# Kernel optimization log

Measured on AMD Instinct MI355X. Metric: run time of the kernel, lower is better.

Reference implementation:

```python
import jax, jax.numpy as jnp
import numpy as np
import math

B, T1, T2, T3, D = 8, 32, 32, 16, 512
L, DL = 20, 128


def setup_inputs() -> dict:
    key = jax.random.key(0)
    ks = jax.random.split(key, 16)
    s = lambda fan: 1.0 / math.sqrt(fan)
    return {
        "f_c": jax.random.normal(ks[0], (B, T1, T2, T3, D), jnp.float32),
        "f_w": jax.random.normal(ks[1], (B, L, D), jnp.float32),
        "f_s": jax.random.normal(ks[2], (B, D), jnp.float32),
        "f_m": jax.random.normal(ks[3], (B, T1, T2, D), jnp.float32),
        "Wc_down": jax.random.normal(ks[4], (DL, D), jnp.float32) * s(D),
        "bc_down": jnp.zeros((DL,), jnp.float32),
        "Ww": jax.random.normal(ks[5], (DL, D), jnp.float32) * s(D),
        "bw": jnp.zeros((DL,), jnp.float32),
        "Ws": jax.random.normal(ks[6], (DL, D), jnp.float32) * s(D),
        "bs": jnp.zeros((DL,), jnp.float32),
        "Wq": jax.random.normal(ks[7], (DL, DL), jnp.float32) * s(DL),
        "bq": jnp.zeros((DL,), jnp.float32),
        "Wk": jax.random.normal(ks[8], (DL, DL), jnp.float32) * s(DL),
        "bk": jnp.zeros((DL,), jnp.float32),
        "Wc_up": jax.random.normal(ks[9], (D, DL), jnp.float32) * s(DL),
        "bc_up": jnp.zeros((D,), jnp.float32),
    }


def reference(f_c, f_w, f_s, f_m, Wc_down, bc_down, Ww, bw, Ws, bs,
              Wq, bq, Wk, bk, Wc_up, bc_up):
    inv_sqrt_dl = 1.0 / math.sqrt(DL)
    # 1x1 conv projections == per-position linear layers
    f_c_hat = jnp.einsum('bxyzd,ld->bxyzl', f_c, Wc_down) + bc_down  # [B,T1,T2,T3,dl]
    f_w_hat = f_w @ Ww.T + bw                                        # [B,L,dl]
    f_s_hat = f_s @ Ws.T + bs                                        # [B,dl]
    # Content attention: query from map, key/value from words
    q = f_c_hat @ Wq.T + bq                                          # [B,T1,T2,T3,dl]
    k = f_w_hat @ Wk.T + bk                                          # [B,L,dl]
    scores = jnp.einsum('bxyzd,bld->bxyzl', q, k) * inv_sqrt_dl
    attn = jax.nn.softmax(scores, axis=-1)
    f_caq = jnp.einsum('bxyzl,bld->bxyzd', attn, f_w_hat)            # [B,T1,T2,T3,dl]
    # Gate with sentence feature
    f_cq = f_c_hat * (f_caq + f_s_hat[:, None, None, None, :])
    # Self-attention over last spatial axis (T3)
    A_c = jnp.einsum('bxyzd,bxywd->bxyzw', f_cq, f_cq) * inv_sqrt_dl  # [B,T1,T2,T3,T3]
    A_c = jax.nn.softmax(A_c, axis=-1)
    f_cc_hat = jnp.einsum('bxyzw,bxywd->bxyzd', A_c, f_c_hat)
    f_cc = jnp.einsum('bxyzl,dl->bxyzd', f_cc_hat, Wc_up) + bc_up     # [B,T1,T2,T3,D]
    # Sigmoid gating residual for f_m
    g_m = jax.nn.sigmoid(f_m * f_s[:, None, None, :])
    fbar_m = g_m * f_m                                                # [B,T1,T2,D]
    return f_cc + f_c + fbar_m[:, :, :, None, :]
```

## Files before the change

kernel.cpp:

```cpp
#include <hip/hip_runtime.h>
#include <math.h>

#define B_ 8
#define T1_ 32
#define T2_ 32
#define T3_ 16
#define D_ 512
#define L_ 20
#define DL_ 128
#define M_ (B_*T1_*T2_*T3_)
#define ROWS 64

#define WS_FW   0
#define WS_KQ   20480
#define WS_FS   40960
#define WS_SB   41984
#define WS_WDB  42144
#define WS_WUB  74912

typedef __attribute__((ext_vector_type(8))) short short8_t;
typedef __attribute__((ext_vector_type(4))) float f32x4;

__device__ __forceinline__ unsigned short f2b(float f) {
  unsigned int u = __float_as_uint(f);
  return (unsigned short)((u + 0x7fffu + ((u >> 16) & 1u)) >> 16);
}
__device__ __forceinline__ float b2f(short s) {
  return __uint_as_float(((unsigned)(unsigned short)s) << 16);
}
__device__ __forceinline__ int4 pack8(float4 a, float4 b) {
  int4 p;
  p.x = (int)f2b(a.x) | ((int)f2b(a.y) << 16);
  p.y = (int)f2b(a.z) | ((int)f2b(a.w) << 16);
  p.z = (int)f2b(b.x) | ((int)f2b(b.y) << 16);
  p.w = (int)f2b(b.z) | ((int)f2b(b.w) << 16);
  return p;
}

__global__ __launch_bounds__(256) void k0_convert(
    const float* __restrict__ Wd, const float* __restrict__ Wu,
    unsigned short* __restrict__ wdb, unsigned short* __restrict__ wub) {
  int g = blockIdx.x * 256 + threadIdx.x;
  if (g < 16384) {
    float4 v = ((const float4*)Wd)[g];
    ushort4 h; h.x = f2b(v.x); h.y = f2b(v.y); h.z = f2b(v.z); h.w = f2b(v.w);
    ((ushort4*)wdb)[g] = h;
  } else {
    int q = g - 16384;
    float4 v = ((const float4*)Wu)[q];
    ushort4 h; h.x = f2b(v.x); h.y = f2b(v.y); h.z = f2b(v.z); h.w = f2b(v.w);
    ((ushort4*)wub)[q] = h;
  }
}

__global__ __launch_bounds__(128) void k1_small(
    const float* __restrict__ f_w, const float* __restrict__ f_s,
    const float* __restrict__ Ww, const float* __restrict__ bw,
    const float* __restrict__ Ws, const float* __restrict__ bs,
    const float* __restrict__ Wq, const float* __restrict__ bq,
    const float* __restrict__ Wk, const float* __restrict__ bk,
    float* __restrict__ ws) {
  const int bl = blockIdx.x;
  const int b = bl / L_, l = bl % L_;
  const int d = threadIdx.x;
  __shared__ float s_fw[DL_];
  __shared__ float s_k[DL_];
  {
    const float* x = f_w + (size_t)(b*L_+l)*D_;
    const float* w = Ww + (size_t)d*D_;
    float acc = 0.f;
    for (int i = 0; i < D_; i += 4)
      acc += x[i]*w[i] + x[i+1]*w[i+1] + x[i+2]*w[i+2] + x[i+3]*w[i+3];
    acc += bw[d];
    s_fw[d] = acc;
    ws[WS_FW + (b*L_+l)*DL_ + d] = acc;
  }
  if (l == 0) {
    const float* x = f_s + (size_t)b*D_;
    const float* w = Ws + (size_t)d*D_;
    float acc = 0.f;
    for (int i = 0; i < D_; i += 4)
      acc += x[i]*w[i] + x[i+1]*w[i+1] + x[i+2]*w[i+2] + x[i+3]*w[i+3];
    ws[WS_FS + b*DL_ + d] = acc + bs[d];
  }
  __syncthreads();
  {
    const float* w = Wk + (size_t)d*DL_;
    float acc = 0.f;
    for (int i = 0; i < DL_; ++i) acc += s_fw[i]*w[i];
    s_k[d] = acc + bk[d];
  }
  __syncthreads();
  {
    float acc = 0.f;
    for (int c = 0; c < DL_; ++c) acc += s_k[c] * Wq[c*DL_ + d];
    ws[WS_KQ + (b*L_+l)*DL_ + d] = acc;
  }
  if (d == 0) {
    float acc = 0.f;
    for (int c = 0; c < DL_; ++c) acc += bq[c]*s_k[c];
    ws[WS_SB + b*L_ + l] = acc;
  }
}

#define SFCH_B 0
#define FCQ_B  16384
#define WD0_B  32768
#define WD1_B  49152
#define FC0_B  65536
#define FC1_B  73728
#define KQ_B   32768
#define FWT_B  40960
#define ATB_B  49152
#define ATTN_B 57344
#define WU0_B  32768
#define WU1_B  49152
#define SB_B   76960
#define FS_B   77056
#define AC_B   77568
#define SMEM_B 81920

__global__ __launch_bounds__(512, 4) void k2_fused(
    const float* __restrict__ f_c, const unsigned short* __restrict__ wdb,
    const unsigned short* __restrict__ wub,
    const float* __restrict__ bc_down, const float* __restrict__ bc_up,
    const float* __restrict__ f_m, const float* __restrict__ f_s,
    const float* __restrict__ ws, float* __restrict__ out) {
  __shared__ __align__(16) char smb[SMEM_B];
  float* sAttn = (float*)(smb + ATTN_B);
  float* sAc   = (float*)(smb + AC_B);
  float* sFs   = (float*)(smb + FS_B);
  float* sSb   = (float*)(smb + SB_B);

  const int t = threadIdx.x;
  const int row0 = blockIdx.x * ROWS;
  const int b = row0 >> 14;
  const int lane = t & 63, w = t >> 6;
  const int l15 = lane & 15, l4 = lane >> 4;
  const float inv_sqrt_dl = 0.08838834764831843f;
  const f32x4 z4 = {0.f, 0.f, 0.f, 0.f};

  const int sd_r  = t >> 3;
  const int sd_k8 = (t & 7) * 8;
  const int sd_swz = (sd_k8 * 2) ^ ((sd_r & 7) << 4);

  f32x4 dacc[4];
  #pragma unroll
  for (int rt = 0; rt < 4; ++rt) dacc[rt] = z4;

  {
    const unsigned short* wp = wdb + sd_k8;
    int4 wrA = *(const int4*)(wp + (size_t)sd_r * D_);
    int4 wrB = *(const int4*)(wp + (size_t)(sd_r + 64) * D_);
    const float* src = f_c + (size_t)(row0 + sd_r) * D_ + sd_k8;
    float4 v0 = *(const float4*)src;
    float4 v1 = *(const float4*)(src + 4);
    *(int4*)(smb + WD0_B + sd_r * 128 + sd_swz) = wrA;
    *(int4*)(smb + WD0_B + (sd_r + 64) * 128 + sd_swz) = wrB;
    *(int4*)(smb + FC0_B + sd_r * 128 + sd_swz) = pack8(v0, v1);
  }
  __syncthreads();

  {
    char* cur_wd = smb + WD0_B; char* nxt_wd = smb + WD1_B;
    char* cur_fc = smb + FC0_B; char* nxt_fc = smb + FC1_B;
    const int ad = w * 16 + l15;
    const int aswz = (ad & 7) << 4;
    for (int ch = 0; ch < 8; ++ch) {
      int4 wrA, wrB; float4 v0, v1;
      if (ch < 7) {
        const int kn = (ch + 1) * 64;
        const unsigned short* wp = wdb + kn + sd_k8;
        wrA = *(const int4*)(wp + (size_t)sd_r * D_);
        wrB = *(const int4*)(wp + (size_t)(sd_r + 64) * D_);
        const float* src = f_c + (size_t)(row0 + sd_r) * D_ + kn + sd_k8;
        v0 = *(const float4*)src; v1 = *(const float4*)(src + 4);
      }
      #pragma unroll
      for (int ks = 0; ks < 2; ++ks) {
        short8_t afrag = *(const short8_t*)(cur_wd + ad * 128 +
                          ((ks*64 + l4*16) ^ aswz));
        #pragma unroll
        for (int rt = 0; rt < 4; ++rt) {
          const int rr = rt*16 + l15;
          short8_t bfrag = *(const short8_t*)(cur_fc + rr * 128 +
                            ((ks*64 + l4*16) ^ ((rr & 7) << 4)));
          dacc[rt] = __builtin_amdgcn_mfma_f32_16x16x32_bf16(afrag, bfrag, dacc[rt], 0, 0, 0);
        }
      }
      if (ch < 7) {
        *(int4*)(nxt_wd + sd_r * 128 + sd_swz) = wrA;
        *(int4*)(nxt_wd + (sd_r + 64) * 128 + sd_swz) = wrB;
        *(int4*)(nxt_fc + sd_r * 128 + sd_swz) = pack8(v0, v1);
      }
      __syncthreads();
      char* tw = cur_wd; cur_wd = nxt_wd; nxt_wd = tw;
      char* tf = cur_fc; cur_fc = nxt_fc; nxt_fc = tf;
    }
  }
  {
    const int d0 = w*16 + l4*4;
    float4 bias = *(const float4*)(bc_down + d0);
    #pragma unroll
    for (int rt = 0; rt < 4; ++rt) {
      const int rr = rt*16 + l15;
      ushort4 pk;
      pk.x = f2b(dacc[rt][0] + bias.x); pk.y = f2b(dacc[rt][1] + bias.y);
      pk.z = f2b(dacc[rt][2] + bias.z); pk.w = f2b(dacc[rt][3] + bias.w);
      *(ushort4*)(smb + SFCH_B + rr*256 + ((d0*2) ^ ((rr & 7) << 4))) = pk;
    }
  }
  {
    const int l = t >> 4, k8 = (t & 15) * 8;
    int4 v = {0,0,0,0};
    if (l < L_) {
      float4 a0 = *(const float4*)(ws + WS_KQ + (b*L_+l)*DL_ + k8);
      float4 a1 = *(const float4*)(ws + WS_KQ + (b*L_+l)*DL_ + k8 + 4);
      v = pack8(a0, a1);
    }
    *(int4*)(smb + KQ_B + l*256 + ((k8*2) ^ ((l & 7) << 4))) = v;
  }
  {
    const int d = t >> 2, l8 = (t & 3) * 8;
    float vv[8];
    #pragma unroll
    for (int e = 0; e < 8; ++e) {
      const int l = l8 + e;
      vv[e] = (l < L_) ? ws[WS_FW + (b*L_+l)*DL_ + d] : 0.f;
    }
    int4 v;
    v.x = (int)f2b(vv[0]) | ((int)f2b(vv[1]) << 16);
    v.y = (int)f2b(vv[2]) | ((int)f2b(vv[3]) << 16);
    v.z = (int)f2b(vv[4]) | ((int)f2b(vv[5]) << 16);
    v.w = (int)f2b(vv[6]) | ((int)f2b(vv[7]) << 16);
    *(int4*)(smb + FWT_B + d*64 + ((l8*2) ^ ((d & 3) << 4))) = v;
  }
  if (t < 32) *(float4*)(sFs + t*4) = *(const float4*)(ws + WS_FS + b*DL_ + t*4);
  if (t < L_) sSb[t] = ws[WS_SB + b*L_ + t];
  __syncthreads();

  {
    const int lt = w & 1, rt2 = w >> 1;
    const int arow = lt*16 + l15;
    const int brow = rt2*16 + l15;
    f32x4 sacc = z4;
    #pragma unroll
    for (int ks = 0; ks < 4; ++ks) {
      short8_t af = *(const short8_t*)(smb + KQ_B + arow*256 +
                     ((ks*64 + l4*16) ^ ((arow & 7) << 4)));
      short8_t bf = *(const short8_t*)(smb + SFCH_B + brow*256 +
                     ((ks*64 + l4*16) ^ ((brow & 7) << 4)));
      sacc = __builtin_amdgcn_mfma_f32_16x16x32_bf16(af, bf, sacc, 0, 0, 0);
    }
    const int r2 = rt2*16 + l15;
    #pragma unroll
    for (int reg = 0; reg < 4; ++reg) {
      const int lval = lt*16 + l4*4 + reg;
      if (lval < L_) sAttn[r2*21 + lval] = (sacc[reg] + sSb[lval]) * inv_sqrt_dl;
    }
  }
  __syncthreads();
  if (t < ROWS) {
    float* srow = sAttn + t*21;
    float m = -1e30f;
    for (int l = 0; l < L_; ++l) m = fmaxf(m, srow[l]);
    float sum = 0.f;
    for (int l = 0; l < L_; ++l) { float e = __expf(srow[l]-m); srow[l] = e; sum += e; }
    float inv = 1.f/sum;
    for (int l = 0; l < L_; ++l) srow[l] *= inv;
  }
  __syncthreads();
  {
    const int r = t >> 3, k8 = (t & 7) * 8;
    int4 v = {0,0,0,0};
    if (k8 < L_) {
      float vv[8];
      #pragma unroll
      for (int e = 0; e < 8; ++e) {
        const int l = k8 + e;
        vv[e] = (l < L_) ? sAttn[r*21 + l] : 0.f;
      }
      v.x = (int)f2b(vv[0]) | ((int)f2b(vv[1]) << 16);
      v.y = (int)f2b(vv[2]) | ((int)f2b(vv[3]) << 16);
      v.z = (int)f2b(vv[4]) | ((int)f2b(vv[5]) << 16);
      v.w = (int)f2b(vv[6]) | ((int)f2b(vv[7]) << 16);
    }
    *(int4*)(smb + ATB_B + r*128 + ((k8*2) ^ ((r & 7) << 4))) = v;
  }
  __syncthreads();
  {
    f32x4 cacc[4];
    #pragma unroll
    for (int rt = 0; rt < 4; ++rt) cacc[rt] = z4;
    const int arow = w*16 + l15;
    short8_t af = *(const short8_t*)(smb + FWT_B + arow*64 +
                   ((l4*16) ^ ((arow & 3) << 4)));
    #pragma unroll
    for (int rt = 0; rt < 4; ++rt) {
      const int brow = rt*16 + l15;
      short8_t bf = *(const short8_t*)(smb + ATB_B + brow*128 +
                     ((l4*16) ^ ((brow & 7) << 4)));
      cacc[rt] = __builtin_amdgcn_mfma_f32_16x16x32_bf16(af, bf, cacc[rt], 0, 0, 0);
    }
    const int d0 = w*16 + l4*4;
    float4 fs4 = *(const float4*)(sFs + d0);
    #pragma unroll
    for (int rt = 0; rt < 4; ++rt) {
      const int r = rt*16 + l15;
      const int rs = (r & 7) << 4;
      ushort4 fh = *(const ushort4*)(smb + SFCH_B + r*256 + ((d0*2) ^ rs));
      ushort4 pk;
      pk.x = f2b(b2f((short)fh.x)*(cacc[rt][0] + fs4.x));
      pk.y = f2b(b2f((short)fh.y)*(cacc[rt][1] + fs4.y));
      pk.z = f2b(b2f((short)fh.z)*(cacc[rt][2] + fs4.z));
      pk.w = f2b(b2f((short)fh.w)*(cacc[rt][3] + fs4.w));
      *(ushort4*)(smb + FCQ_B + r*256 + ((d0*2) ^ rs)) = pk;
    }
  }
  __syncthreads();
  if (w < 4) {
    const int zrow = w*16 + l15;
    f32x4 pacc = z4;
    #pragma unroll
    for (int ks = 0; ks < 4; ++ks) {
      short8_t fq = *(const short8_t*)(smb + FCQ_B + zrow*256 +
                     ((ks*64 + l4*16) ^ ((zrow & 7) << 4)));
      pacc = __builtin_amdgcn_mfma_f32_16x16x32_bf16(fq, fq, pacc, 0, 0, 0);
    }
    float p0[4], m[4], e[4], s[4];
    #pragma unroll
    for (int reg = 0; reg < 4; ++reg) p0[reg] = pacc[reg] * inv_sqrt_dl;
    #pragma unroll
    for (int reg = 0; reg < 4; ++reg) {
      m[reg] = p0[reg];
      m[reg] = fmaxf(m[reg], __shfl_xor(m[reg], 1));
      m[reg] = fmaxf(m[reg], __shfl_xor(m[reg], 2));
      m[reg] = fmaxf(m[reg], __shfl_xor(m[reg], 4));
      m[reg] = fmaxf(m[reg], __shfl_xor(m[reg], 8));
      e[reg] = __expf(p0[reg] - m[reg]);
      s[reg] = e[reg];
      s[reg] += __shfl_xor(s[reg], 1);
      s[reg] += __shfl_xor(s[reg], 2);
      s[reg] += __shfl_xor(s[reg], 4);
      s[reg] += __shfl_xor(s[reg], 8);
    }
    #pragma unroll
    for (int reg = 0; reg < 4; ++reg)
      sAc[(w*16 + l4*4 + reg)*17 + l15] = e[reg] / s[reg];
  }
  __syncthreads();

  const int su_d = t >> 4;
  const int su_k8 = (t & 15) * 8;
  const int su_swz = (su_k8 * 2) ^ ((su_d & 7) << 4);
  int4 u0, u1;
  {
    const unsigned short* up = wub + su_k8;
    u0 = *(const int4*)(up + (size_t)su_d * DL_);
    u1 = *(const int4*)(up + (size_t)(su_d + 32) * DL_);
  }
  for (int p = t; p < ROWS*32; p += 512) {
    const int r = p >> 5, d4 = (p & 31)*4;
    const int g = r >> 4, z = r & 15;
    float ax = 0.f, ay = 0.f, az = 0.f, aw = 0.f;
    #pragma unroll
    for (int wq = 0; wq < 16; ++wq) {
      float a = sAc[(g*16+z)*17 + wq];
      const int fr = g*16 + wq;
      ushort4 fv = *(const ushort4*)(smb + SFCH_B + fr*256 + ((d4*2) ^ ((fr & 7) << 4)));
      ax += a*b2f((short)fv.x); ay += a*b2f((short)fv.y);
      az += a*b2f((short)fv.z); aw += a*b2f((short)fv.w);
    }
    ushort4 pk;
    pk.x = f2b(ax); pk.y = f2b(ay); pk.z = f2b(az); pk.w = f2b(aw);
    *(ushort4*)(smb + FCQ_B + r*256 + ((d4*2) ^ ((r & 7) << 4))) = pk;
  }
  *(int4*)(smb + WU0_B + su_d * 256 + su_swz) = u0;
  *(int4*)(smb + WU0_B + (su_d + 32) * 256 + su_swz) = u1;
  __syncthreads();

  {
    char* cur_wu = smb + WU0_B; char* nxt_wu = smb + WU1_B;
    const int ad = (w & 3)*16 + l15;
    const int aswz = (ad & 7) << 4;
    const int rbase = (w >> 2) * 32;
    for (int ch = 0; ch < 8; ++ch) {
      if (ch < 7) {
        const unsigned short* up = wub + (size_t)(ch + 1)*64*DL_ + su_k8;
        u0 = *(const int4*)(up + (size_t)su_d * DL_);
        u1 = *(const int4*)(up + (size_t)(su_d + 32) * DL_);
      }
      f32x4 uacc[2]; uacc[0] = z4; uacc[1] = z4;
      #pragma unroll
      for (int ks = 0; ks < 4; ++ks) {
        short8_t afrag = *(const short8_t*)(cur_wu + ad*256 +
                          ((ks*64 + l4*16) ^ aswz));
        #pragma unroll
        for (int cf = 0; cf < 2; ++cf) {
          const int rr = rbase + cf*16 + l15;
          short8_t bfrag = *(const short8_t*)(smb + FCQ_B + rr*256 +
                            ((ks*64 + l4*16) ^ ((rr & 7) << 4)));
          uacc[cf] = __builtin_amdgcn_mfma_f32_16x16x32_bf16(afrag, bfrag, uacc[cf], 0, 0, 0);
        }
      }
      {
        const int d0 = ch*64 + (w & 3)*16 + l4*4;
        float4 bias = *(const float4*)(bc_up + d0);
        float4 fs4 = *(const float4*)(f_s + (size_t)b*D_ + d0);
        #pragma unroll
        for (int cf = 0; cf < 2; ++cf) {
          const int grow = row0 + rbase + cf*16 + l15;
          const size_t obase = (size_t)grow * D_;
          float4 fm4 = *(const float4*)(f_m + ((size_t)(grow >> 4))*D_ + d0);
          float4 fc4 = *(const float4*)(f_c + obase + d0);
          float4 o;
          o.x = uacc[cf][0] + bias.x + fc4.x + fm4.x/(1.f + __expf(-fm4.x*fs4.x));
          o.y = uacc[cf][1] + bias.y + fc4.y + fm4.y/(1.f + __expf(-fm4.y*fs4.y));
          o.z = uacc[cf][2] + bias.z + fc4.z + fm4.z/(1.f + __expf(-fm4.z*fs4.z));
          o.w = uacc[cf][3] + bias.w + fc4.w + fm4.w/(1.f + __expf(-fm4.w*fs4.w));
          *(float4*)(out + obase + d0) = o;
        }
      }
      if (ch < 7) {
        *(int4*)(nxt_wu + su_d * 256 + su_swz) = u0;
        *(int4*)(nxt_wu + (su_d + 32) * 256 + su_swz) = u1;
      }
      __syncthreads();
      char* tu = cur_wu; cur_wu = nxt_wu; nxt_wu = tu;
    }
  }
}

extern "C" void kernel_launch(void* const* d_in, const int* in_sizes, int n_in,
                              void* d_out, int out_size, void* d_ws, size_t ws_size,
                              hipStream_t stream) {
  (void)in_sizes; (void)n_in; (void)out_size; (void)ws_size;
  const float* f_c     = (const float*)d_in[0];
  const float* f_w     = (const float*)d_in[1];
  const float* f_s     = (const float*)d_in[2];
  const float* f_m     = (const float*)d_in[3];
  const float* Wc_down = (const float*)d_in[4];
  const float* bc_down = (const float*)d_in[5];
  const float* Ww      = (const float*)d_in[6];
  const float* bw      = (const float*)d_in[7];
  const float* Ws      = (const float*)d_in[8];
  const float* bs      = (const float*)d_in[9];
  const float* Wq      = (const float*)d_in[10];
  const float* bq      = (const float*)d_in[11];
  const float* Wk      = (const float*)d_in[12];
  const float* bk      = (const float*)d_in[13];
  const float* Wc_up   = (const float*)d_in[14];
  const float* bc_up   = (const float*)d_in[15];
  float* out = (float*)d_out;
  float* wsf = (float*)d_ws;
  unsigned short* wdb = (unsigned short*)(wsf + WS_WDB);
  unsigned short* wub = (unsigned short*)(wsf + WS_WUB);

  hipLaunchKernelGGL(k0_convert, dim3(128), dim3(256), 0, stream,
                     Wc_down, Wc_up, wdb, wub);
  hipLaunchKernelGGL(k1_small, dim3(B_*L_), dim3(128), 0, stream,
                     f_w, f_s, Ww, bw, Ws, bs, Wq, bq, Wk, bk, wsf);
  hipLaunchKernelGGL(k2_fused, dim3(M_/ROWS), dim3(512), 0, stream,
                     f_c, wdb, wub, bc_down, bc_up, f_m, f_s, wsf, out);
}
```

Baseline: 245.2 us.

## Split fused kernel into down-projection, attention, and up-projection kernels

The single fused kernel is split into three kernels: a down-projection GEMM writing bf16 f_c_hat to workspace, a mid kernel doing content attention and T3 self-attention in place on that buffer, and an up-projection kernel with the residual epilogue. Precomputed K·Wq and transposed f_w_hat are now stored as bf16 in global memory, so MFMA fragments load directly from global instead of being staged in LDS. Each kernel uses far less shared memory, which is meant to allow higher occupancy. The cost is an extra global round trip of the 128-wide intermediate, roughly 32 MB of bf16 traffic, plus two more kernel launches.

```diff
diff --git a/kernel.cpp b/kernel.cpp
--- a/kernel.cpp
+++ b/kernel.cpp
@@ -9,14 +9,14 @@
 #define L_ 20
 #define DL_ 128
 #define M_ (B_*T1_*T2_*T3_)
-#define ROWS 64
-
-#define WS_FW   0
-#define WS_KQ   20480
-#define WS_FS   40960
-#define WS_SB   41984
-#define WS_WDB  42144
-#define WS_WUB  74912
+
+#define WS_FS   0
+#define WS_SB   1024
+#define WS_WDB  1184
+#define WS_WUB  33952
+#define WS_KQB  66720
+#define WS_FWT  83104
+#define WS_FCH  99488
 
 typedef __attribute__((ext_vector_type(8))) short short8_t;
 typedef __attribute__((ext_vector_type(4))) float f32x4;
@@ -39,7 +39,8 @@
 
 __global__ __launch_bounds__(256) void k0_convert(
     const float* __restrict__ Wd, const float* __restrict__ Wu,
-    unsigned short* __restrict__ wdb, unsigned short* __restrict__ wub) {
+    unsigned short* __restrict__ wdb, unsigned short* __restrict__ wub,
+    unsigned short* __restrict__ kqb, unsigned short* __restrict__ fwtb) {
   int g = blockIdx.x * 256 + threadIdx.x;
   if (g < 16384) {
     float4 v = ((const float4*)Wd)[g];
@@ -51,6 +52,8 @@
     ushort4 h; h.x = f2b(v.x); h.y = f2b(v.y); h.z = f2b(v.z); h.w = f2b(v.w);
     ((ushort4*)wub)[q] = h;
   }
+  kqb[g]  = 0;
+  fwtb[g] = 0;
 }
 
 __global__ __launch_bounds__(128) void k1_small(
@@ -59,6 +62,7 @@
     const float* __restrict__ Ws, const float* __restrict__ bs,
     const float* __restrict__ Wq, const float* __restrict__ bq,
     const float* __restrict__ Wk, const float* __restrict__ bk,
+    unsigned short* __restrict__ kqb, unsigned short* __restrict__ fwtb,
     float* __restrict__ ws) {
   const int bl = blockIdx.x;
   const int b = bl / L_, l = bl % L_;
@@ -73,7 +77,7 @@
       acc += x[i]*w[i] + x[i+1]*w[i+1] + x[i+2]*w[i+2] + x[i+3]*w[i+3];
     acc += bw[d];
     s_fw[d] = acc;
-    ws[WS_FW + (b*L_+l)*DL_ + d] = acc;
+    fwtb[((size_t)(b*DL_ + d))*32 + l] = f2b(acc);
   }
   if (l == 0) {
     const float* x = f_s + (size_t)b*D_;
@@ -94,7 +98,7 @@
   {
     float acc = 0.f;
     for (int c = 0; c < DL_; ++c) acc += s_k[c] * Wq[c*DL_ + d];
-    ws[WS_KQ + (b*L_+l)*DL_ + d] = acc;
+    kqb[((size_t)(b*32 + l))*DL_ + d] = f2b(acc);
   }
   if (d == 0) {
     float acc = 0.f;
@@ -103,41 +107,20 @@
   }
 }
 
-#define SFCH_B 0
-#define FCQ_B  16384
-#define WD0_B  32768
-#define WD1_B  49152
-#define FC0_B  65536
-#define FC1_B  73728
-#define KQ_B   32768
-#define FWT_B  40960
-#define ATB_B  49152
-#define ATTN_B 57344
-#define WU0_B  32768
-#define WU1_B  49152
-#define SB_B   76960
-#define FS_B   77056
-#define AC_B   77568
-#define SMEM_B 81920
-
-__global__ __launch_bounds__(512, 4) void k2_fused(
+#define KA_WD0 0
+#define KA_WD1 16384
+#define KA_FC0 32768
+#define KA_FC1 40960
+#define KA_SMEM 49152
+
+__global__ __launch_bounds__(512, 6) void kA_down(
     const float* __restrict__ f_c, const unsigned short* __restrict__ wdb,
-    const unsigned short* __restrict__ wub,
-    const float* __restrict__ bc_down, const float* __restrict__ bc_up,
-    const float* __restrict__ f_m, const float* __restrict__ f_s,
-    const float* __restrict__ ws, float* __restrict__ out) {
-  __shared__ __align__(16) char smb[SMEM_B];
-  float* sAttn = (float*)(smb + ATTN_B);
-  float* sAc   = (float*)(smb + AC_B);
-  float* sFs   = (float*)(smb + FS_B);
-  float* sSb   = (float*)(smb + SB_B);
-
+    const float* __restrict__ bc_down, unsigned short* __restrict__ fch) {
+  __shared__ __align__(16) char smb[KA_SMEM];
   const int t = threadIdx.x;
-  const int row0 = blockIdx.x * ROWS;
-  const int b = row0 >> 14;
+  const int row0 = blockIdx.x * 64;
   const int lane = t & 63, w = t >> 6;
   const int l15 = lane & 15, l4 = lane >> 4;
-  const float inv_sqrt_dl = 0.08838834764831843f;
   const f32x4 z4 = {0.f, 0.f, 0.f, 0.f};
 
   const int sd_r  = t >> 3;
@@ -155,15 +138,15 @@
     const float* src = f_c + (size_t)(row0 + sd_r) * D_ + sd_k8;
     float4 v0 = *(const float4*)src;
     float4 v1 = *(const float4*)(src + 4);
-    *(int4*)(smb + WD0_B + sd_r * 128 + sd_swz) = wrA;
-    *(int4*)(smb + WD0_B + (sd_r + 64) * 128 + sd_swz) = wrB;
-    *(int4*)(smb + FC0_B + sd_r * 128 + sd_swz) = pack8(v0, v1);
-  }
-  __syncthreads();
-
-  {
-    char* cur_wd = smb + WD0_B; char* nxt_wd = smb + WD1_B;
-    char* cur_fc = smb + FC0_B; char* nxt_fc = smb + FC1_B;
+    *(int4*)(smb + KA_WD0 + sd_r * 128 + sd_swz) = wrA;
+    *(int4*)(smb + KA_WD0 + (sd_r + 64) * 128 + sd_swz) = wrB;
+    *(int4*)(smb + KA_FC0 + sd_r * 128 + sd_swz) = pack8(v0, v1);
+  }
+  __syncthreads();
+
+  {
+    char* cur_wd = smb + KA_WD0; char* nxt_wd = smb + KA_WD1;
+    char* cur_fc = smb + KA_FC0; char* nxt_fc = smb + KA_FC1;
     const int ad = w * 16 + l15;
     const int aswz = (ad & 7) << 4;
     for (int ch = 0; ch < 8; ++ch) {
@@ -207,33 +190,43 @@
       ushort4 pk;
       pk.x = f2b(dacc[rt][0] + bias.x); pk.y = f2b(dacc[rt][1] + bias.y);
       pk.z = f2b(dacc[rt][2] + bias.z); pk.w = f2b(dacc[rt][3] + bias.w);
-      *(ushort4*)(smb + SFCH_B + rr*256 + ((d0*2) ^ ((rr & 7) << 4))) = pk;
-    }
-  }
-  {
-    const int l = t >> 4, k8 = (t & 15) * 8;
-    int4 v = {0,0,0,0};
-    if (l < L_) {
-      float4 a0 = *(const float4*)(ws + WS_KQ + (b*L_+l)*DL_ + k8);
-      float4 a1 = *(const float4*)(ws + WS_KQ + (b*L_+l)*DL_ + k8 + 4);
-      v = pack8(a0, a1);
-    }
-    *(int4*)(smb + KQ_B + l*256 + ((k8*2) ^ ((l & 7) << 4))) = v;
-  }
-  {
-    const int d = t >> 2, l8 = (t & 3) * 8;
-    float vv[8];
-    #pragma unroll
-    for (int e = 0; e < 8; ++e) {
-      const int l = l8 + e;
-      vv[e] = (l < L_) ? ws[WS_FW + (b*L_+l)*DL_ + d] : 0.f;
-    }
-    int4 v;
-    v.x = (int)f2b(vv[0]) | ((int)f2b(vv[1]) << 16);
-    v.y = (int)f2b(vv[2]) | ((int)f2b(vv[3]) << 16);
-    v.z = (int)f2b(vv[4]) | ((int)f2b(vv[5]) << 16);
-    v.w = (int)f2b(vv[6]) | ((int)f2b(vv[7]) << 16);
-    *(int4*)(smb + FWT_B + d*64 + ((l8*2) ^ ((d & 3) << 4))) = v;
+      *(ushort4*)(fch + (size_t)(row0 + rr)*DL_ + d0) = pk;
+    }
+  }
+}
+
+#define KB_SFCH 0
+#define KB_FCQ  8192
+#define KB_ATB  16384
+#define KB_ATTN 20480
+#define KB_AC   23168
+#define KB_FS   25344
+#define KB_SB   25856
+#define KB_SMEM 25984
+
+__global__ __launch_bounds__(256, 6) void kB_mid(
+    unsigned short* __restrict__ fch, const unsigned short* __restrict__ kqb,
+    const unsigned short* __restrict__ fwtb, const float* __restrict__ ws) {
+  __shared__ __align__(16) char smb[KB_SMEM];
+  float* sAttn = (float*)(smb + KB_ATTN);
+  float* sAc   = (float*)(smb + KB_AC);
+  float* sFs   = (float*)(smb + KB_FS);
+  float* sSb   = (float*)(smb + KB_SB);
+
+  const int t = threadIdx.x;
+  const int row0 = blockIdx.x * 32;
+  const int b = row0 >> 14;
+  const int lane = t & 63, w = t >> 6;
+  const int l15 = lane & 15, l4 = lane >> 4;
+  const float inv_sqrt_dl = 0.08838834764831843f;
+  const f32x4 z4 = {0.f, 0.f, 0.f, 0.f};
+
+  #pragma unroll
+  for (int i = 0; i < 2; ++i) {
+    const int f4 = t + i*256;
+    const int r = f4 >> 4, k8 = (f4 & 15) * 8;
+    int4 v = *(const int4*)(fch + (size_t)(row0 + r)*DL_ + k8);
+    *(int4*)(smb + KB_SFCH + r*256 + ((k8*2) ^ ((r & 7) << 4))) = v;
   }
   if (t < 32) *(float4*)(sFs + t*4) = *(const float4*)(ws + WS_FS + b*DL_ + t*4);
   if (t < L_) sSb[t] = ws[WS_SB + b*L_ + t];
@@ -243,12 +236,12 @@
     const int lt = w & 1, rt2 = w >> 1;
     const int arow = lt*16 + l15;
     const int brow = rt2*16 + l15;
+    const unsigned short* kqrow = kqb + (size_t)(b*32 + arow)*DL_;
     f32x4 sacc = z4;
     #pragma unroll
     for (int ks = 0; ks < 4; ++ks) {
-      short8_t af = *(const short8_t*)(smb + KQ_B + arow*256 +
-                     ((ks*64 + l4*16) ^ ((arow & 7) << 4)));
-      short8_t bf = *(const short8_t*)(smb + SFCH_B + brow*256 +
+      short8_t af = *(const short8_t*)(kqrow + ks*32 + l4*8);
+      short8_t bf = *(const short8_t*)(smb + KB_SFCH + brow*256 +
                      ((ks*64 + l4*16) ^ ((brow & 7) << 4)));
       sacc = __builtin_amdgcn_mfma_f32_16x16x32_bf16(af, bf, sacc, 0, 0, 0);
     }
@@ -260,7 +253,7 @@
     }
   }
   __syncthreads();
-  if (t < ROWS) {
+  if (t < 32) {
     float* srow = sAttn + t*21;
     float m = -1e30f;
     for (int l = 0; l < L_; ++l) m = fmaxf(m, srow[l]);
@@ -285,45 +278,48 @@
       v.z = (int)f2b(vv[4]) | ((int)f2b(vv[5]) << 16);
       v.w = (int)f2b(vv[6]) | ((int)f2b(vv[7]) << 16);
     }
-    *(int4*)(smb + ATB_B + r*128 + ((k8*2) ^ ((r & 7) << 4))) = v;
-  }
-  __syncthreads();
-  {
-    f32x4 cacc[4];
-    #pragma unroll
-    for (int rt = 0; rt < 4; ++rt) cacc[rt] = z4;
-    const int arow = w*16 + l15;
-    short8_t af = *(const short8_t*)(smb + FWT_B + arow*64 +
-                   ((l4*16) ^ ((arow & 3) << 4)));
-    #pragma unroll
-    for (int rt = 0; rt < 4; ++rt) {
-      const int brow = rt*16 + l15;
-      short8_t bf = *(const short8_t*)(smb + ATB_B + brow*128 +
-                     ((l4*16) ^ ((brow & 7) << 4)));
-      cacc[rt] = __builtin_amdgcn_mfma_f32_16x16x32_bf16(af, bf, cacc[rt], 0, 0, 0);
-    }
-    const int d0 = w*16 + l4*4;
-    float4 fs4 = *(const float4*)(sFs + d0);
-    #pragma unroll
-    for (int rt = 0; rt < 4; ++rt) {
+    *(int4*)(smb + KB_ATB + r*128 + ((k8*2) ^ ((r & 7) << 4))) = v;
+  }
+  __syncthreads();
+  {
+    f32x4 cacc[2][2];
+    cacc[0][0] = z4; cacc[0][1] = z4; cacc[1][0] = z4; cacc[1][1] = z4;
+    #pragma unroll
+    for (int dt = 0; dt < 2; ++dt) {
+      const int arow = (w*2 + dt)*16 + l15;
+      short8_t af = *(const short8_t*)(fwtb + (size_t)(b*DL_ + arow)*32 + l4*8);
+      #pragma unroll
+      for (int rt = 0; rt < 2; ++rt) {
+        const int brow = rt*16 + l15;
+        short8_t bf = *(const short8_t*)(smb + KB_ATB + brow*128 +
+                       ((l4*16) ^ ((brow & 7) << 4)));
+        cacc[dt][rt] = __builtin_amdgcn_mfma_f32_16x16x32_bf16(af, bf, cacc[dt][rt], 0, 0, 0);
+      }
+    }
+    #pragma unroll
+    for (int dt = 0; dt < 2; ++dt)
+    #pragma unroll
+    for (int rt = 0; rt < 2; ++rt) {
+      const int d0 = (w*2 + dt)*16 + l4*4;
       const int r = rt*16 + l15;
       const int rs = (r & 7) << 4;
-      ushort4 fh = *(const ushort4*)(smb + SFCH_B + r*256 + ((d0*2) ^ rs));
+      float4 fs4 = *(const float4*)(sFs + d0);
+      ushort4 fh = *(const ushort4*)(smb + KB_SFCH + r*256 + ((d0*2) ^ rs));
       ushort4 pk;
-      pk.x = f2b(b2f((short)fh.x)*(cacc[rt][0] + fs4.x));
-      pk.y = f2b(b2f((short)fh.y)*(cacc[rt][1] + fs4.y));
-      pk.z = f2b(b2f((short)fh.z)*(cacc[rt][2] + fs4.z));
-      pk.w = f2b(b2f((short)fh.w)*(cacc[rt][3] + fs4.w));
-      *(ushort4*)(smb + FCQ_B + r*256 + ((d0*2) ^ rs)) = pk;
-    }
-  }
-  __syncthreads();
-  if (w < 4) {
+      pk.x = f2b(b2f((short)fh.x)*(cacc[dt][rt][0] + fs4.x));
+      pk.y = f2b(b2f((short)fh.y)*(cacc[dt][rt][1] + fs4.y));
+      pk.z = f2b(b2f((short)fh.z)*(cacc[dt][rt][2] + fs4.z));
+      pk.w = f2b(b2f((short)fh.w)*(cacc[dt][rt][3] + fs4.w));
+      *(ushort4*)(smb + KB_FCQ + r*256 + ((d0*2) ^ rs)) = pk;
+    }
+  }
+  __syncthreads();
+  if (w < 2) {
     const int zrow = w*16 + l15;
     f32x4 pacc = z4;
     #pragma unroll
     for (int ks = 0; ks < 4; ++ks) {
-      short8_t fq = *(const short8_t*)(smb + FCQ_B + zrow*256 +
+      short8_t fq = *(const short8_t*)(smb + KB_FCQ + zrow*256 +
                      ((ks*64 + l4*16) ^ ((zrow & 7) << 4)));
       pacc = __builtin_amdgcn_mfma_f32_16x16x32_bf16(fq, fq, pacc, 0, 0, 0);
     }
@@ -349,42 +345,61 @@
       sAc[(w*16 + l4*4 + reg)*17 + l15] = e[reg] / s[reg];
   }
   __syncthreads();
+  for (int p = t; p < 1024; p += 256) {
+    const int r = p >> 5, d4 = (p & 31)*4;
+    const int g = r >> 4, z = r & 15;
+    float ax = 0.f, ay = 0.f, az = 0.f, aw = 0.f;
+    #pragma unroll
+    for (int wq = 0; wq < 16; ++wq) {
+      float a = sAc[(g*16+z)*17 + wq];
+      const int fr = g*16 + wq;
+      ushort4 fv = *(const ushort4*)(smb + KB_SFCH + fr*256 + ((d4*2) ^ ((fr & 7) << 4)));
+      ax += a*b2f((short)fv.x); ay += a*b2f((short)fv.y);
+      az += a*b2f((short)fv.z); aw += a*b2f((short)fv.w);
+    }
+    ushort4 pk;
+    pk.x = f2b(ax); pk.y = f2b(ay); pk.z = f2b(az); pk.w = f2b(aw);
+    *(ushort4*)(fch + (size_t)(row0 + r)*DL_ + d4) = pk;
+  }
+}
+
+#define KC_WU0 0
+#define KC_WU1 16384
+#define KC_SMEM 32768
+
+__global__ __launch_bounds__(512, 8) void kC_up(
+    const unsigned short* __restrict__ fcc, const unsigned short* __restrict__ wub,
+    const float* __restrict__ bc_up, const float* __restrict__ f_c,
+    const float* __restrict__ f_m, const float* __restrict__ f_s,
+    float* __restrict__ out) {
+  __shared__ __align__(16) char smb[KC_SMEM];
+  const int t = threadIdx.x;
+  const int row0 = blockIdx.x * 64;
+  const int b = row0 >> 14;
+  const int lane = t & 63, w = t >> 6;
+  const int l15 = lane & 15, l4 = lane >> 4;
+  const f32x4 z4 = {0.f, 0.f, 0.f, 0.f};
 
   const int su_d = t >> 4;
   const int su_k8 = (t & 15) * 8;
   const int su_swz = (su_k8 * 2) ^ ((su_d & 7) << 4);
-  int4 u0, u1;
+
   {
     const unsigned short* up = wub + su_k8;
-    u0 = *(const int4*)(up + (size_t)su_d * DL_);
-    u1 = *(const int4*)(up + (size_t)(su_d + 32) * DL_);
-  }
-  for (int p = t; p < ROWS*32; p += 512) {
-    const int r = p >> 5, d4 = (p & 31)*4;
-    const int g = r >> 4, z = r & 15;
-    float ax = 0.f, ay = 0.f, az = 0.f, aw = 0.f;
-    #pragma unroll
-    for (int wq = 0; wq < 16; ++wq) {
-      float a = sAc[(g*16+z)*17 + wq];
-      const int fr = g*16 + wq;
-      ushort4 fv = *(const ushort4*)(smb + SFCH_B + fr*256 + ((d4*2) ^ ((fr & 7) << 4)));
-      ax += a*b2f((short)fv.x); ay += a*b2f((short)fv.y);
-      az += a*b2f((short)fv.z); aw += a*b2f((short)fv.w);
-    }
-    ushort4 pk;
-    pk.x = f2b(ax); pk.y = f2b(ay); pk.z = f2b(az); pk.w = f2b(aw);
-    *(ushort4*)(smb + FCQ_B + r*256 + ((d4*2) ^ ((r & 7) << 4))) = pk;
-  }
-  *(int4*)(smb + WU0_B + su_d * 256 + su_swz) = u0;
-  *(int4*)(smb + WU0_B + (su_d + 32) * 256 + su_swz) = u1;
-  __syncthreads();
-
-  {
-    char* cur_wu = smb + WU0_B; char* nxt_wu = smb + WU1_B;
+    int4 u0 = *(const int4*)(up + (size_t)su_d * DL_);
+    int4 u1 = *(const int4*)(up + (size_t)(su_d + 32) * DL_);
+    *(int4*)(smb + KC_WU0 + su_d * 256 + su_swz) = u0;
+    *(int4*)(smb + KC_WU0 + (su_d + 32) * 256 + su_swz) = u1;
+  }
+  __syncthreads();
+
+  {
+    char* cur_wu = smb + KC_WU0; char* nxt_wu = smb + KC_WU1;
     const int ad = (w & 3)*16 + l15;
     const int aswz = (ad & 7) << 4;
     const int rbase = (w >> 2) * 32;
     for (int ch = 0; ch < 8; ++ch) {
+      int4 u0, u1;
       if (ch < 7) {
         const unsigned short* up = wub + (size_t)(ch + 1)*64*DL_ + su_k8;
         u0 = *(const int4*)(up + (size_t)su_d * DL_);
@@ -398,8 +413,8 @@
         #pragma unroll
         for (int cf = 0; cf < 2; ++cf) {
           const int rr = rbase + cf*16 + l15;
-          short8_t bfrag = *(const short8_t*)(smb + FCQ_B + rr*256 +
-                            ((ks*64 + l4*16) ^ ((rr & 7) << 4)));
+          short8_t bfrag = *(const short8_t*)(fcc + (size_t)(row0 + rr)*DL_ +
+                            ks*32 + l4*8);
           uacc[cf] = __builtin_amdgcn_mfma_f32_16x16x32_bf16(afrag, bfrag, uacc[cf], 0, 0, 0);
         }
       }
@@ -453,13 +468,20 @@
   const float* bc_up   = (const float*)d_in[15];
   float* out = (float*)d_out;
   float* wsf = (float*)d_ws;
-  unsigned short* wdb = (unsigned short*)(wsf + WS_WDB);
-  unsigned short* wub = (unsigned short*)(wsf + WS_WUB);
+  unsigned short* wdb  = (unsigned short*)(wsf + WS_WDB);
+  unsigned short* wub  = (unsigned short*)(wsf + WS_WUB);
+  unsigned short* kqb  = (unsigned short*)(wsf + WS_KQB);
+  unsigned short* fwtb = (unsigned short*)(wsf + WS_FWT);
+  unsigned short* fch  = (unsigned short*)(wsf + WS_FCH);
 
   hipLaunchKernelGGL(k0_convert, dim3(128), dim3(256), 0, stream,
-                     Wc_down, Wc_up, wdb, wub);
+                     Wc_down, Wc_up, wdb, wub, kqb, fwtb);
   hipLaunchKernelGGL(k1_small, dim3(B_*L_), dim3(128), 0, stream,
-                     f_w, f_s, Ww, bw, Ws, bs, Wq, bq, Wk, bk, wsf);
-  hipLaunchKernelGGL(k2_fused, dim3(M_/ROWS), dim3(512), 0, stream,
-                     f_c, wdb, wub, bc_down, bc_up, f_m, f_s, wsf, out);
-}
+                     f_w, f_s, Ww, bw, Ws, bs, Wq, bq, Wk, bk, kqb, fwtb, wsf);
+  hipLaunchKernelGGL(kA_down, dim3(M_/64), dim3(512), 0, stream,
+                     f_c, wdb, bc_down, fch);
+  hipLaunchKernelGGL(kB_mid, dim3(M_/32), dim3(256), 0, stream,
+                     fch, kqb, fwtb, wsf);
+  hipLaunchKernelGGL(kC_up, dim3(M_/64), dim3(512), 0, stream,
+                     fch, wub, bc_up, f_c, f_m, f_s, out);
+}
```

Result: slower. 484.8 us (+97.7%).

## Shrink k2 shared memory by removing double buffers and precomputing bf16 KQ/FWT

Applied to the files above, without the earlier changes.

Removes the double buffering of the down and up projection weight and f_c tiles, and aliases shared regions so the fused kernel needs 48KB of LDS instead of 80KB. Launch bounds rise from 4 to 6 blocks per CU. The small kernel now writes KQ and the transposed f_w_hat directly as padded bf16 in global memory, and the main kernel reads its MFMA fragments from there instead of staging them in LDS. In exchange, global loads are no longer overlapped with MFMA inside each block, and every chunk pays an extra synchronisation. The change relies on higher occupancy to hide that latency instead.

```diff
diff --git a/kernel.cpp b/kernel.cpp
--- a/kernel.cpp
+++ b/kernel.cpp
@@ -11,12 +11,12 @@
 #define M_ (B_*T1_*T2_*T3_)
 #define ROWS 64
 
-#define WS_FW   0
-#define WS_KQ   20480
-#define WS_FS   40960
-#define WS_SB   41984
-#define WS_WDB  42144
-#define WS_WUB  74912
+#define WS_FS   0
+#define WS_SB   1024
+#define WS_WDB  1184
+#define WS_WUB  33952
+#define WS_KQB  66720
+#define WS_FWT  83104
 
 typedef __attribute__((ext_vector_type(8))) short short8_t;
 typedef __attribute__((ext_vector_type(4))) float f32x4;
@@ -39,7 +39,8 @@
 
 __global__ __launch_bounds__(256) void k0_convert(
     const float* __restrict__ Wd, const float* __restrict__ Wu,
-    unsigned short* __restrict__ wdb, unsigned short* __restrict__ wub) {
+    unsigned short* __restrict__ wdb, unsigned short* __restrict__ wub,
+    unsigned short* __restrict__ kqb, unsigned short* __restrict__ fwtb) {
   int g = blockIdx.x * 256 + threadIdx.x;
   if (g < 16384) {
     float4 v = ((const float4*)Wd)[g];
@@ -51,6 +52,8 @@
     ushort4 h; h.x = f2b(v.x); h.y = f2b(v.y); h.z = f2b(v.z); h.w = f2b(v.w);
     ((ushort4*)wub)[q] = h;
   }
+  kqb[g]  = 0;
+  fwtb[g] = 0;
 }
 
 __global__ __launch_bounds__(128) void k1_small(
@@ -59,6 +62,7 @@
     const float* __restrict__ Ws, const float* __restrict__ bs,
     const float* __restrict__ Wq, const float* __restrict__ bq,
     const float* __restrict__ Wk, const float* __restrict__ bk,
+    unsigned short* __restrict__ kqb, unsigned short* __restrict__ fwtb,
     float* __restrict__ ws) {
   const int bl = blockIdx.x;
   const int b = bl / L_, l = bl % L_;
@@ -73,7 +77,7 @@
       acc += x[i]*w[i] + x[i+1]*w[i+1] + x[i+2]*w[i+2] + x[i+3]*w[i+3];
     acc += bw[d];
     s_fw[d] = acc;
-    ws[WS_FW + (b*L_+l)*DL_ + d] = acc;
+    fwtb[((size_t)(b*DL_ + d))*32 + l] = f2b(acc);
   }
   if (l == 0) {
     const float* x = f_s + (size_t)b*D_;
@@ -94,7 +98,7 @@
   {
     float acc = 0.f;
     for (int c = 0; c < DL_; ++c) acc += s_k[c] * Wq[c*DL_ + d];
-    ws[WS_KQ + (b*L_+l)*DL_ + d] = acc;
+    kqb[((size_t)(b*32 + l))*DL_ + d] = f2b(acc);
   }
   if (d == 0) {
     float acc = 0.f;
@@ -105,29 +109,26 @@
 
 #define SFCH_B 0
 #define FCQ_B  16384
-#define WD0_B  32768
-#define WD1_B  49152
-#define FC0_B  65536
-#define FC1_B  73728
-#define KQ_B   32768
-#define FWT_B  40960
-#define ATB_B  49152
-#define ATTN_B 57344
-#define WU0_B  32768
-#define WU1_B  49152
-#define SB_B   76960
-#define FS_B   77056
-#define AC_B   77568
-#define SMEM_B 81920
-
-__global__ __launch_bounds__(512, 4) void k2_fused(
+#define FC_B   FCQ_B
+#define ATTN_F FCQ_B
+#define R3_B   32768
+#define WD_B   R3_B
+#define ATB_B  R3_B
+#define AC_B   (R3_B + 8192)
+#define FS_B   (R3_B + 12800)
+#define SB_B   (R3_B + 13312)
+#define WU_B   R3_B
+#define SMEM_B 49152
+
+__global__ __launch_bounds__(512, 6) void k2_fused(
     const float* __restrict__ f_c, const unsigned short* __restrict__ wdb,
     const unsigned short* __restrict__ wub,
+    const unsigned short* __restrict__ kqb, const unsigned short* __restrict__ fwtb,
     const float* __restrict__ bc_down, const float* __restrict__ bc_up,
     const float* __restrict__ f_m, const float* __restrict__ f_s,
     const float* __restrict__ ws, float* __restrict__ out) {
   __shared__ __align__(16) char smb[SMEM_B];
-  float* sAttn = (float*)(smb + ATTN_B);
+  float* sAttn = (float*)(smb + ATTN_F);
   float* sAc   = (float*)(smb + AC_B);
   float* sFs   = (float*)(smb + FS_B);
   float* sSb   = (float*)(smb + SB_B);
@@ -149,53 +150,37 @@
   for (int rt = 0; rt < 4; ++rt) dacc[rt] = z4;
 
   {
-    const unsigned short* wp = wdb + sd_k8;
-    int4 wrA = *(const int4*)(wp + (size_t)sd_r * D_);
-    int4 wrB = *(const int4*)(wp + (size_t)(sd_r + 64) * D_);
-    const float* src = f_c + (size_t)(row0 + sd_r) * D_ + sd_k8;
-    float4 v0 = *(const float4*)src;
-    float4 v1 = *(const float4*)(src + 4);
-    *(int4*)(smb + WD0_B + sd_r * 128 + sd_swz) = wrA;
-    *(int4*)(smb + WD0_B + (sd_r + 64) * 128 + sd_swz) = wrB;
-    *(int4*)(smb + FC0_B + sd_r * 128 + sd_swz) = pack8(v0, v1);
-  }
-  __syncthreads();
-
-  {
-    char* cur_wd = smb + WD0_B; char* nxt_wd = smb + WD1_B;
-    char* cur_fc = smb + FC0_B; char* nxt_fc = smb + FC1_B;
     const int ad = w * 16 + l15;
     const int aswz = (ad & 7) << 4;
     for (int ch = 0; ch < 8; ++ch) {
-      int4 wrA, wrB; float4 v0, v1;
-      if (ch < 7) {
-        const int kn = (ch + 1) * 64;
-        const unsigned short* wp = wdb + kn + sd_k8;
-        wrA = *(const int4*)(wp + (size_t)sd_r * D_);
-        wrB = *(const int4*)(wp + (size_t)(sd_r + 64) * D_);
-        const float* src = f_c + (size_t)(row0 + sd_r) * D_ + kn + sd_k8;
-        v0 = *(const float4*)src; v1 = *(const float4*)(src + 4);
-      }
+      const int kc = ch * 64;
+      #pragma unroll
+      for (int i = 0; i < 2; ++i) {
+        const int idx = t + i*512;
+        const int r = idx >> 3, k8 = (idx & 7) * 8;
+        *(int4*)(smb + WD_B + r*128 + ((k8*2) ^ ((r & 7) << 4))) =
+          *(const int4*)(wdb + (size_t)r*D_ + kc + k8);
+      }
+      {
+        const float* src = f_c + (size_t)(row0 + sd_r)*D_ + kc + sd_k8;
+        float4 v0 = *(const float4*)src;
+        float4 v1 = *(const float4*)(src + 4);
+        *(int4*)(smb + FC_B + sd_r*128 + sd_swz) = pack8(v0, v1);
+      }
+      __syncthreads();
       #pragma unroll
       for (int ks = 0; ks < 2; ++ks) {
-        short8_t afrag = *(const short8_t*)(cur_wd + ad * 128 +
+        short8_t afrag = *(const short8_t*)(smb + WD_B + ad*128 +
                           ((ks*64 + l4*16) ^ aswz));
         #pragma unroll
         for (int rt = 0; rt < 4; ++rt) {
           const int rr = rt*16 + l15;
-          short8_t bfrag = *(const short8_t*)(cur_fc + rr * 128 +
+          short8_t bfrag = *(const short8_t*)(smb + FC_B + rr*128 +
                             ((ks*64 + l4*16) ^ ((rr & 7) << 4)));
           dacc[rt] = __builtin_amdgcn_mfma_f32_16x16x32_bf16(afrag, bfrag, dacc[rt], 0, 0, 0);
         }
       }
-      if (ch < 7) {
-        *(int4*)(nxt_wd + sd_r * 128 + sd_swz) = wrA;
-        *(int4*)(nxt_wd + (sd_r + 64) * 128 + sd_swz) = wrB;
-        *(int4*)(nxt_fc + sd_r * 128 + sd_swz) = pack8(v0, v1);
-      }
       __syncthreads();
-      char* tw = cur_wd; cur_wd = nxt_wd; nxt_wd = tw;
-      char* tf = cur_fc; cur_fc = nxt_fc; nxt_fc = tf;
     }
   }
   {
@@ -210,31 +195,6 @@
       *(ushort4*)(smb + SFCH_B + rr*256 + ((d0*2) ^ ((rr & 7) << 4))) = pk;
     }
   }
-  {
-    const int l = t >> 4, k8 = (t & 15) * 8;
-    int4 v = {0,0,0,0};
-    if (l < L_) {
-      float4 a0 = *(const float4*)(ws + WS_KQ + (b*L_+l)*DL_ + k8);
-      float4 a1 = *(const float4*)(ws + WS_KQ + (b*L_+l)*DL_ + k8 + 4);
-      v = pack8(a0, a1);
-    }
-    *(int4*)(smb + KQ_B + l*256 + ((k8*2) ^ ((l & 7) << 4))) = v;
-  }
-  {
-    const int d = t >> 2, l8 = (t & 3) * 8;
-    float vv[8];
-    #pragma unroll
-    for (int e = 0; e < 8; ++e) {
-      const int l = l8 + e;
-      vv[e] = (l < L_) ? ws[WS_FW + (b*L_+l)*DL_ + d] : 0.f;
-    }
-    int4 v;
-    v.x = (int)f2b(vv[0]) | ((int)f2b(vv[1]) << 16);
-    v.y = (int)f2b(vv[2]) | ((int)f2b(vv[3]) << 16);
-    v.z = (int)f2b(vv[4]) | ((int)f2b(vv[5]) << 16);
-    v.w = (int)f2b(vv[6]) | ((int)f2b(vv[7]) << 16);
-    *(int4*)(smb + FWT_B + d*64 + ((l8*2) ^ ((d & 3) << 4))) = v;
-  }
   if (t < 32) *(float4*)(sFs + t*4) = *(const float4*)(ws + WS_FS + b*DL_ + t*4);
   if (t < L_) sSb[t] = ws[WS_SB + b*L_ + t];
   __syncthreads();
@@ -243,11 +203,11 @@
     const int lt = w & 1, rt2 = w >> 1;
     const int arow = lt*16 + l15;
     const int brow = rt2*16 + l15;
+    const unsigned short* kqrow = kqb + (size_t)(b*32 + arow)*DL_;
     f32x4 sacc = z4;
     #pragma unroll
     for (int ks = 0; ks < 4; ++ks) {
-      short8_t af = *(const short8_t*)(smb + KQ_B + arow*256 +
-                     ((ks*64 + l4*16) ^ ((arow & 7) << 4)));
+      short8_t af = *(const short8_t*)(kqrow + ks*32 + l4*8);
       short8_t bf = *(const short8_t*)(smb + SFCH_B + brow*256 +
                      ((ks*64 + l4*16) ^ ((brow & 7) << 4)));
       sacc = __builtin_amdgcn_mfma_f32_16x16x32_bf16(af, bf, sacc, 0, 0, 0);
@@ -293,8 +253,7 @@
     #pragma unroll
     for (int rt = 0; rt < 4; ++rt) cacc[rt] = z4;
     const int arow = w*16 + l15;
-    short8_t af = *(const short8_t*)(smb + FWT_B + arow*64 +
-                   ((l4*16) ^ ((arow & 3) << 4)));
+    short8_t af = *(const short8_t*)(fwtb + (size_t)(b*DL_ + arow)*32 + l4*8);
     #pragma unroll
     for (int rt = 0; rt < 4; ++rt) {
       const int brow = rt*16 + l15;
@@ -349,16 +308,6 @@
       sAc[(w*16 + l4*4 + reg)*17 + l15] = e[reg] / s[reg];
   }
   __syncthreads();
-
-  const int su_d = t >> 4;
-  const int su_k8 = (t & 15) * 8;
-  const int su_swz = (su_k8 * 2) ^ ((su_d & 7) << 4);
-  int4 u0, u1;
-  {
-    const unsigned short* up = wub + su_k8;
-    u0 = *(const int4*)(up + (size_t)su_d * DL_);
-    u1 = *(const int4*)(up + (size_t)(su_d + 32) * DL_);
-  }
   for (int p = t; p < ROWS*32; p += 512) {
     const int r = p >> 5, d4 = (p & 31)*4;
     const int g = r >> 4, z = r & 15;
@@ -375,25 +324,28 @@
     pk.x = f2b(ax); pk.y = f2b(ay); pk.z = f2b(az); pk.w = f2b(aw);
     *(ushort4*)(smb + FCQ_B + r*256 + ((d4*2) ^ ((r & 7) << 4))) = pk;
   }
-  *(int4*)(smb + WU0_B + su_d * 256 + su_swz) = u0;
-  *(int4*)(smb + WU0_B + (su_d + 32) * 256 + su_swz) = u1;
-  __syncthreads();
-
-  {
-    char* cur_wu = smb + WU0_B; char* nxt_wu = smb + WU1_B;
+  __syncthreads();
+
+  {
+    const int su_d = t >> 4;
+    const int su_k8 = (t & 15) * 8;
+    const int su_swz = (su_k8 * 2) ^ ((su_d & 7) << 4);
     const int ad = (w & 3)*16 + l15;
     const int aswz = (ad & 7) << 4;
     const int rbase = (w >> 2) * 32;
     for (int ch = 0; ch < 8; ++ch) {
-      if (ch < 7) {
-        const unsigned short* up = wub + (size_t)(ch + 1)*64*DL_ + su_k8;
-        u0 = *(const int4*)(up + (size_t)su_d * DL_);
-        u1 = *(const int4*)(up + (size_t)(su_d + 32) * DL_);
-      }
+      {
+        const unsigned short* up = wub + (size_t)ch*64*DL_ + su_k8;
+        int4 u0 = *(const int4*)(up + (size_t)su_d * DL_);
+        int4 u1 = *(const int4*)(up + (size_t)(su_d + 32) * DL_);
+        *(int4*)(smb + WU_B + su_d * 256 + su_swz) = u0;
+        *(int4*)(smb + WU_B + (su_d + 32) * 256 + su_swz) = u1;
+      }
+      __syncthreads();
       f32x4 uacc[2]; uacc[0] = z4; uacc[1] = z4;
       #pragma unroll
       for (int ks = 0; ks < 4; ++ks) {
-        short8_t afrag = *(const short8_t*)(cur_wu + ad*256 +
+        short8_t afrag = *(const short8_t*)(smb + WU_B + ad*256 +
                           ((ks*64 + l4*16) ^ aswz));
         #pragma unroll
         for (int cf = 0; cf < 2; ++cf) {
@@ -421,12 +373,7 @@
           *(float4*)(out + obase + d0) = o;
         }
       }
-      if (ch < 7) {
-        *(int4*)(nxt_wu + su_d * 256 + su_swz) = u0;
-        *(int4*)(nxt_wu + (su_d + 32) * 256 + su_swz) = u1;
-      }
       __syncthreads();
-      char* tu = cur_wu; cur_wu = nxt_wu; nxt_wu = tu;
     }
   }
 }
@@ -453,13 +400,15 @@
   const float* bc_up   = (const float*)d_in[15];
   float* out = (float*)d_out;
   float* wsf = (float*)d_ws;
-  unsigned short* wdb = (unsigned short*)(wsf + WS_WDB);
-  unsigned short* wub = (unsigned short*)(wsf + WS_WUB);
+  unsigned short* wdb  = (unsigned short*)(wsf + WS_WDB);
+  unsigned short* wub  = (unsigned short*)(wsf + WS_WUB);
+  unsigned short* kqb  = (unsigned short*)(wsf + WS_KQB);
+  unsigned short* fwtb = (unsigned short*)(wsf + WS_FWT);
 
   hipLaunchKernelGGL(k0_convert, dim3(128), dim3(256), 0, stream,
-                     Wc_down, Wc_up, wdb, wub);
+                     Wc_down, Wc_up, wdb, wub, kqb, fwtb);
   hipLaunchKernelGGL(k1_small, dim3(B_*L_), dim3(128), 0, stream,
-                     f_w, f_s, Ww, bw, Ws, bs, Wq, bq, Wk, bk, wsf);
+                     f_w, f_s, Ww, bw, Ws, bs, Wq, bq, Wk, bk, kqb, fwtb, wsf);
   hipLaunchKernelGGL(k2_fused, dim3(M_/ROWS), dim3(512), 0, stream,
-                     f_c, wdb, wub, bc_down, bc_up, f_m, f_s, wsf, out);
-}
+                     f_c, wdb, wub, kqb, fwtb, bc_down, bc_up, f_m, f_s, wsf, out);
+}
```

Result: no change. 243.5 us (-0.7%).
